# Kernel tuning notes

Measured on AMD Instinct MI355X. Metric: run time of the kernel, lower is better.

The kernel has to match this reference:

```python
import jax, jax.numpy as jnp
import numpy as np

D = 1024          # n_embd
H = 4 * D         # SwiGLU hidden
E = 8             # num_experts
K = 2             # top_k
B, T = 2, 2048

def setup_inputs() -> dict:
    key = jax.random.key(0)
    ks = jax.random.split(key, 12)
    s = 0.02
    return {
        "x":   jax.random.normal(ks[0], (B, T, D), jnp.float32),
        "noise": jax.random.normal(ks[1], (B, T, E), jnp.float32),
        # router (nn.Linear with bias=True by default)
        "Wr": jax.random.normal(ks[2], (D, E), jnp.float32) * s,
        "br": jnp.zeros((E,), jnp.float32),
        "Wn": jax.random.normal(ks[3], (D, E), jnp.float32) * s,
        "bn": jnp.zeros((E,), jnp.float32),
        # routed experts, stacked over E (bias=False)
        "Wg": jax.random.normal(ks[4], (E, D, H), jnp.float32) * s,
        "Wu": jax.random.normal(ks[5], (E, D, H), jnp.float32) * s,
        "Wd": jax.random.normal(ks[6], (E, H, D), jnp.float32) * s,
        # shared expert (num_shared_experts = 1)
        "Sg": jax.random.normal(ks[7], (D, H), jnp.float32) * s,
        "Su": jax.random.normal(ks[8], (D, H), jnp.float32) * s,
        "Sd": jax.random.normal(ks[9], (H, D), jnp.float32) * s,
    }

def reference(x, noise, Wr, br, Wn, bn, Wg, Wu, Wd, Sg, Su, Sd):
    # shared expert: SwiGLU MLP over all tokens
    shared_out = (jax.nn.silu(x @ Sg) * (x @ Su)) @ Sd  # [B,T,D]

    # noisy top-k router
    logits = x @ Wr + br                                 # [B,T,E]
    noise_logits = x @ Wn + bn
    noisy = logits + noise * jax.nn.softplus(noise_logits)
    _, top_idx = jax.lax.top_k(noisy, K)                 # [B,T,K]
    sel = jax.nn.one_hot(top_idx, E, dtype=noisy.dtype).sum(-2) > 0  # [B,T,E]
    sparse = jnp.where(sel, noisy, -jnp.inf)
    gates = jax.nn.softmax(sparse, axis=-1)              # [B,T,E], 0 for unselected

    # original runs every expert densely over all tokens, weighted by gate
    g = jnp.einsum('btd,edh->beth', x, Wg)               # [B,E,T,H]
    u = jnp.einsum('btd,edh->beth', x, Wu)
    y = jnp.einsum('beth,ehd->betd', jax.nn.silu(g) * u, Wd)  # [B,E,T,D]
    routed = jnp.einsum('bte,betd->btd', gates, y)

    return shared_out + routed
```

## Files before the change

kernel.cpp:

```cpp
#include <hip/hip_runtime.h>

typedef unsigned short u16;
typedef unsigned int u32;
typedef __attribute__((ext_vector_type(8))) __bf16 bf16x8;
typedef __attribute__((ext_vector_type(4))) float f32x4;

#define D_ 1024
#define H_ 4096
#define E_ 8
#define NT_ 4096
#define RCAP_ 8704

#define LDSH_ 8192
#define LDST_ 16384


__device__ __forceinline__ u16 f2b(float f) {
  u32 u = __float_as_uint(f);
  u += 0x7fffu + ((u >> 16) & 1u);
  return (u16)(u >> 16);
}

__device__ __forceinline__ void glds16(const u16* g, u16* l) {
  __builtin_amdgcn_global_load_lds((const __attribute__((address_space(1))) void*)g,
                                   (__attribute__((address_space(3))) void*)l, 16, 0, 0);
}

__device__ __forceinline__ void stage_half(const u16* __restrict__ g, u16* l, int wv, int lane) {
#pragma unroll
  for (int c = 0; c < 2; ++c)
    glds16(g + c * 4096 + wv * 512 + lane * 8, l + c * 4096 + wv * 512);
}

__global__ void init_ints(int* p, int n) {
  int i = threadIdx.x;
  if (i < n) p[i] = 0;
}

__global__ void pack_x(const float* __restrict__ x, u16* __restrict__ xp) {
  const int t = blockIdx.x, i = threadIdx.x;
  float4 v = ((const float4*)(x + (size_t)t * D_))[i];
  const int kb = i >> 4, ch = (i >> 1) & 7, sub = (i & 1) * 4;
  u16 tmp[4] = {f2b(v.x), f2b(v.y), f2b(v.z), f2b(v.w)};
  *(uint2*)(xp + ((size_t)kb * NT_ + t) * 64 + ((ch ^ (t & 7)) << 3) + sub) = *(uint2*)tmp;
}

__global__ void pack_b(const float* __restrict__ src, const float* __restrict__ src2,
                       u16* __restrict__ dst, int Kdim, int Rdim) {
  const int r0 = blockIdx.x * 64, k0 = blockIdx.y * 64, z = blockIdx.z;
  const int Rout = src2 ? (Rdim * 2) : Rdim;
  src += (size_t)z * Kdim * Rdim;
  if (src2) src2 += (size_t)z * Kdim * Rdim;
  u16* dkb = dst + (size_t)z * (Kdim >> 6) * Rout * 64 + (size_t)(k0 >> 6) * Rout * 64;
  __shared__ float t1[64][65];
  __shared__ float t2[64][65];
  const int tx = threadIdx.x, ty = threadIdx.y;
#pragma unroll
  for (int i = 0; i < 16; ++i) {
    const int kk = ty + 4 * i;
    t1[kk][tx] = src[(size_t)(k0 + kk) * Rdim + r0 + tx];
    if (src2) t2[kk][tx] = src2[(size_t)(k0 + kk) * Rdim + r0 + tx];
  }
  __syncthreads();
  const int idx = ty * 64 + tx;
  const int ch = idx & 7, rl0 = idx >> 3;
#pragma unroll
  for (int half = 0; half < 2; ++half) {
    const int rl = rl0 + 32 * half;
    const int r = r0 + rl;
    if (src2) {
      const int rg = 32 * (r >> 4) + (r & 15), ru = rg + 16;
      const int kg = (ch ^ (rg & 7)) << 3;
      union { u16 v[8]; uint4 q; } pg, pu;
#pragma unroll
      for (int j = 0; j < 8; ++j) pg.v[j] = f2b(t1[kg + j][rl]);
#pragma unroll
      for (int j = 0; j < 8; ++j) pu.v[j] = f2b(t2[kg + j][rl]);
      *(uint4*)(dkb + (size_t)rg * 64 + ch * 8) = pg.q;
      *(uint4*)(dkb + (size_t)ru * 64 + ch * 8) = pu.q;
    } else {
      const int kc = (ch ^ (r & 7)) << 3;
      union { u16 v[8]; uint4 q; } pk;
#pragma unroll
      for (int j = 0; j < 8; ++j) pk.v[j] = f2b(t1[kc + j][rl]);
      *(uint4*)(dkb + (size_t)r * 64 + ch * 8) = pk.q;
    }
  }
}

__global__ void router_k(const float* __restrict__ x, const float* __restrict__ noise,
                         const float* __restrict__ Wr, const float* __restrict__ br,
                         const float* __restrict__ Wn, const float* __restrict__ bn,
                         int* __restrict__ counts, int* __restrict__ tok_e,
                         float* __restrict__ tok_g) {
  const int t = blockIdx.x;
  const int lane = threadIdx.x;
  float xv[16];
#pragma unroll
  for (int i = 0; i < 16; ++i) xv[i] = x[(size_t)t * D_ + lane + 64 * i];
  float nz[E_];
#pragma unroll
  for (int e = 0; e < E_; ++e) {
    float ar = 0.f, an = 0.f;
#pragma unroll
    for (int i = 0; i < 16; ++i) {
      int d = lane + 64 * i;
      ar += xv[i] * Wr[d * E_ + e];
      an += xv[i] * Wn[d * E_ + e];
    }
#pragma unroll
    for (int o = 32; o > 0; o >>= 1) {
      ar += __shfl_down(ar, o, 64);
      an += __shfl_down(an, o, 64);
    }
    if (lane == 0) {
      float lg = ar + br[e], nl = an + bn[e];
      float sp = (nl > 20.f) ? nl : log1pf(expf(nl));
      nz[e] = lg + noise[(size_t)t * E_ + e] * sp;
    }
  }
  if (lane == 0) {
    int i0 = 0;
#pragma unroll
    for (int e = 1; e < E_; ++e) if (nz[e] > nz[i0]) i0 = e;
    int i1 = (i0 == 0) ? 1 : 0;
#pragma unroll
    for (int e = 0; e < E_; ++e) if (e != i0 && nz[e] > nz[i1]) i1 = e;
    float a = nz[i0], b = nz[i1];
    float m = fmaxf(a, b);
    float ea = expf(a - m), eb = expf(b - m);
    float inv = 1.f / (ea + eb);
    tok_e[2 * t] = i0; tok_e[2 * t + 1] = i1;
    tok_g[2 * t] = ea * inv; tok_g[2 * t + 1] = eb * inv;
    atomicAdd(&counts[i0], 1);
    atomicAdd(&counts[i1], 1);
  }
}

__global__ void scan_k(const int* __restrict__ counts, int* __restrict__ offsets) {
  if (threadIdx.x == 0) {
    int acc = 0;
    for (int e = 0; e < E_; ++e) { offsets[e] = acc; acc += (counts[e] + 7) & ~7; }
    offsets[E_] = acc;
  }
}

__global__ void gather_k(const u16* __restrict__ xp, const int* __restrict__ tok_e,
                         const float* __restrict__ tok_g, const int* __restrict__ offsets,
                         int* __restrict__ cursors, u16* __restrict__ Xallp,
                         int* __restrict__ row_token, float* __restrict__ row_gate) {
  const int t = blockIdx.x;
  __shared__ int rws[2];
  if (threadIdx.x < 2) {
    int e = tok_e[2 * t + threadIdx.x];
    int r = offsets[e] + atomicAdd(&cursors[e], 1);
    row_token[r] = t;
    row_gate[r] = tok_g[2 * t + threadIdx.x];
    rws[threadIdx.x] = r;
  }
  __syncthreads();
  const int r0 = rws[0], r1 = rws[1];
  const int x7 = t & 7;
#pragma unroll
  for (int it = 0; it < 2; ++it) {
    const int u = threadIdx.x + 64 * it;
    const int kb = u >> 3, cs = u & 7;
    uint4 v = *(const uint4*)(xp + ((size_t)kb * NT_ + t) * 64 + (cs << 3));
    const int c = cs ^ x7;
    *(uint4*)(Xallp + ((size_t)kb * RCAP_ + r0) * 64 + ((c ^ (r0 & 7)) << 3)) = v;
    *(uint4*)(Xallp + ((size_t)kb * RCAP_ + r1) * 64 + ((c ^ (r1 & 7)) << 3)) = v;
  }
}

__device__ __forceinline__ void gemm_core8(
    const u16* __restrict__ A, const u16* __restrict__ B,
    size_t aKS, size_t bKS, int NKB,
    u16* As, u16* Bs, f32x4 acc[8][4], int tid) {
  const int lane = tid & 63, wv = tid >> 6;
  const int wr = wv >> 2, wc = wv & 3;
  const int lm = lane & 15, lq = lane >> 4;
  const int c0 = ((lq ^ (lm & 7)) << 4);
  const char* asr = (const char*)As + (wr * 128 + lm) * 128;
  const char* bsr = (const char*)Bs + (wc * 64 + lm) * 128;

  stage_half(A,         As,         wv, lane);
  stage_half(A + LDSH_, As + LDSH_, wv, lane);
  stage_half(B,         Bs,         wv, lane);
  stage_half(B + LDSH_, Bs + LDSH_, wv, lane);
  stage_half(A + aKS,   As + LDST_, wv, lane);
  asm volatile("s_waitcnt vmcnt(2)" ::: "memory");
  __builtin_amdgcn_s_barrier();
  __builtin_amdgcn_sched_barrier(0);

  for (int t = 0; t < NKB; ++t) {
    const int bo = (t & 1) << 15;
    const int ou = ((t & 1) ^ 1) * LDST_;
    bf16x8 a[8], bb[4];
#pragma unroll
    for (int i = 0; i < 8; ++i)
      a[i] = *(const bf16x8*)(asr + bo + i * 2048 + c0);
#pragma unroll
    for (int j = 0; j < 4; ++j)
      bb[j] = *(const bf16x8*)(bsr + bo + j * 2048 + c0);
    if (t + 1 < NKB) stage_half(A + (size_t)(t + 1) * aKS + LDSH_, As + ou + LDSH_, wv, lane);
    asm volatile("s_waitcnt lgkmcnt(8)" ::: "memory");
    __builtin_amdgcn_s_barrier();
    asm volatile("s_waitcnt lgkmcnt(0)" ::: "memory");
    __builtin_amdgcn_sched_barrier(0);
    __builtin_amdgcn_s_setprio(1);
#pragma unroll
    for (int i = 0; i < 4; ++i)
#pragma unroll
      for (int j = 0; j < 4; ++j)
        acc[i][j] = __builtin_amdgcn_mfma_f32_16x16x32_bf16(a[i], bb[j], acc[i][j], 0, 0, 0);
    __builtin_amdgcn_s_setprio(0);
    __builtin_amdgcn_s_barrier();
    if (t + 1 < NKB) stage_half(B + (size_t)(t + 1) * bKS, Bs + ou, wv, lane);
    __builtin_amdgcn_s_barrier();
    __builtin_amdgcn_sched_barrier(0);
    __builtin_amdgcn_s_setprio(1);
#pragma unroll
    for (int i = 0; i < 4; ++i)
#pragma unroll
      for (int j = 0; j < 4; ++j)
        acc[4 + i][j] = __builtin_amdgcn_mfma_f32_16x16x32_bf16(a[4 + i], bb[j], acc[4 + i][j], 0, 0, 0);
    __builtin_amdgcn_s_setprio(0);
    __builtin_amdgcn_s_barrier();
#pragma unroll
    for (int i = 0; i < 8; ++i)
      a[i] = *(const bf16x8*)(asr + bo + i * 2048 + (c0 ^ 64));
#pragma unroll
    for (int j = 0; j < 4; ++j)
      bb[j] = *(const bf16x8*)(bsr + bo + j * 2048 + (c0 ^ 64));
    if (t + 1 < NKB) stage_half(B + (size_t)(t + 1) * bKS + LDSH_, Bs + ou + LDSH_, wv, lane);
    asm volatile("s_waitcnt lgkmcnt(8)" ::: "memory");
    __builtin_amdgcn_s_barrier();
    asm volatile("s_waitcnt lgkmcnt(0)" ::: "memory");
    __builtin_amdgcn_sched_barrier(0);
    __builtin_amdgcn_s_setprio(1);
#pragma unroll
    for (int i = 0; i < 4; ++i)
#pragma unroll
      for (int j = 0; j < 4; ++j)
        acc[i][j] = __builtin_amdgcn_mfma_f32_16x16x32_bf16(a[i], bb[j], acc[i][j], 0, 0, 0);
    __builtin_amdgcn_s_setprio(0);
    __builtin_amdgcn_s_barrier();
    if (t + 2 < NKB) stage_half(A + (size_t)(t + 2) * aKS, As + (bo >> 1), wv, lane);
    __builtin_amdgcn_s_barrier();
    __builtin_amdgcn_sched_barrier(0);
    __builtin_amdgcn_s_setprio(1);
#pragma unroll
    for (int i = 0; i < 4; ++i)
#pragma unroll
      for (int j = 0; j < 4; ++j)
        acc[4 + i][j] = __builtin_amdgcn_mfma_f32_16x16x32_bf16(a[4 + i], bb[j], acc[4 + i][j], 0, 0, 0);
    __builtin_amdgcn_s_setprio(0);
    if (t + 1 < NKB) {
      if (t + 2 < NKB) { asm volatile("s_waitcnt vmcnt(2)" ::: "memory"); }
      else             { asm volatile("s_waitcnt vmcnt(0)" ::: "memory"); }
      __builtin_amdgcn_sched_barrier(0);
      __builtin_amdgcn_s_barrier();
    }
  }
}

__global__ __launch_bounds__(512, 2)
void gemm1_k(const u16* __restrict__ Ap, const u16* __restrict__ Bp, u16* __restrict__ actp,
             const int* __restrict__ neArr, const int* __restrict__ offArr,
             int fixedM, int K, int aRowCap) {
  int bx, by, e;
  if (neArr) {
    const int lid = blockIdx.x + (int)gridDim.x * (blockIdx.y + (int)gridDim.y * blockIdx.z);
    e = lid & 7; const int rest = lid >> 3; bx = rest & 15; by = rest >> 4;
  } else { bx = blockIdx.x; by = blockIdx.y; e = 0; }
  const int ne = neArr ? neArr[e] : fixedM;
  const int m0 = bx * 256;
  if (m0 >= ne) return;
  const int off = offArr ? offArr[e] : 0;
  const int n0 = by * 256;
  const int NKB = K >> 6;
  const u16* A = Ap + (size_t)(off + m0) * 64;
  const u16* B = Bp + ((size_t)e * NKB * 8192 + (size_t)n0) * 64;

  __shared__ __align__(16) u16 As[2 * LDST_], Bs[2 * LDST_];
  f32x4 acc[8][4] = {};
  const int tid = threadIdx.x;
  gemm_core8(A, B, (size_t)aRowCap * 64, (size_t)8192 * 64, NKB, As, Bs, acc, tid);

  const int lane = tid & 63, wv = tid >> 6;
  const int wr = wv >> 2, wc = wv & 3;
  const int lm = lane & 15, lq = lane >> 4;
  const int hb = (n0 + wc * 64) >> 1;
#pragma unroll
  for (int i = 0; i < 8; ++i)
#pragma unroll
    for (int r = 0; r < 4; ++r) {
      const int m = m0 + wr * 128 + i * 16 + lq * 4 + r;
      if (m < ne) {
        const int row = off + m;
        const int r7 = row & 7;
#pragma unroll
        for (int jj = 0; jj < 2; ++jj) {
          float g = acc[i][2 * jj][r], u = acc[i][2 * jj + 1][r];
          float s = g / (1.f + __expf(-g)) * u;
          const int h = hb + jj * 16 + lm;
          actp[((size_t)(h >> 6) * RCAP_ + row) * 64 + ((((h >> 3) & 7) ^ r7) << 3 | (h & 7))] = f2b(s);
        }
      }
    }
}

__global__ __launch_bounds__(512, 2)
void gemm2_k(const u16* __restrict__ Ap, const u16* __restrict__ Bp,
             float* __restrict__ out,
             const int* __restrict__ neArr, const int* __restrict__ offArr,
             const int* __restrict__ row_token, const float* __restrict__ row_gate,
             int fixedM, int K) {
  int bx, by, e;
  if (neArr) {
    const int lid = blockIdx.x + (int)gridDim.x * (blockIdx.y + (int)gridDim.y * blockIdx.z);
    e = lid & 7; const int rest = lid >> 3; bx = rest & 15; by = rest >> 4;
  } else { bx = blockIdx.x; by = blockIdx.y; e = 0; }
  const int ne = neArr ? neArr[e] : fixedM;
  const int m0 = bx * 256;
  if (m0 >= ne) return;
  const int off = offArr ? offArr[e] : 0;
  const int n0 = by * 256;
  const int NKB = K >> 6;
  const u16* A = Ap + (size_t)(off + m0) * 64;
  const u16* B = Bp + ((size_t)e * NKB * 1024 + (size_t)n0) * 64;

  __shared__ __align__(16) u16 As[2 * LDST_], Bs[2 * LDST_];
  f32x4 acc[8][4] = {};
  const int tid = threadIdx.x;
  gemm_core8(A, B, (size_t)RCAP_ * 64, (size_t)1024 * 64, NKB, As, Bs, acc, tid);

  const int lane = tid & 63, wv = tid >> 6;
  const int wr = wv >> 2, wc = wv & 3;
  const int lm = lane & 15, lq = lane >> 4;
#pragma unroll
  for (int i = 0; i < 8; ++i)
#pragma unroll
    for (int r = 0; r < 4; ++r) {
      const int m = m0 + wr * 128 + i * 16 + lq * 4 + r;
      if (m < ne) {
        const int n = n0 + wc * 64 + lm;
        if (row_token) {
          const int tkn = row_token[off + m];
          const float gt = row_gate[off + m];
#pragma unroll
          for (int j = 0; j < 4; ++j)
            atomicAdd(out + (size_t)tkn * D_ + n + j * 16, gt * acc[i][j][r]);
        } else {
#pragma unroll
          for (int j = 0; j < 4; ++j)
            out[(size_t)m * D_ + n + j * 16] = acc[i][j][r];
        }
      }
    }
}

extern "C" void kernel_launch(void* const* d_in, const int* in_sizes, int n_in,
                              void* d_out, int out_size, void* d_ws, size_t ws_size,
                              hipStream_t stream) {
  const float* x     = (const float*)d_in[0];
  const float* noise = (const float*)d_in[1];
  const float* Wr    = (const float*)d_in[2];
  const float* br    = (const float*)d_in[3];
  const float* Wn    = (const float*)d_in[4];
  const float* bn    = (const float*)d_in[5];
  const float* Wg    = (const float*)d_in[6];
  const float* Wu    = (const float*)d_in[7];
  const float* Wd    = (const float*)d_in[8];
  const float* Sg    = (const float*)d_in[9];
  const float* Su    = (const float*)d_in[10];
  const float* Sd    = (const float*)d_in[11];
  float* out = (float*)d_out;

  char* base = (char*)d_ws;
  size_t off = 0;
  auto take = [&](size_t bytes) -> void* {
    void* r = base + off;
    off = (off + bytes + 255) & ~(size_t)255;
    return r;
  };
  u16* Wgup = (u16*)take((size_t)E_ * 16 * 8192 * 64 * 2);
  u16* Wdp  = (u16*)take((size_t)E_ * 64 * 1024 * 64 * 2);
  u16* Sgup = (u16*)take((size_t)16 * 8192 * 64 * 2);
  u16* Sdp  = (u16*)take((size_t)64 * 1024 * 64 * 2);
  u16* xp   = (u16*)take((size_t)16 * NT_ * 64 * 2);
  u16* Xallp = (u16*)take((size_t)16 * RCAP_ * 64 * 2);
  u16* actp  = (u16*)take((size_t)64 * RCAP_ * 64 * 2);
  int*   row_token = (int*)take(RCAP_ * 4);
  float* row_gate  = (float*)take(RCAP_ * 4);
  int*   tok_e = (int*)take(NT_ * 2 * 4);
  float* tok_g = (float*)take(NT_ * 2 * 4);
  int* ints = (int*)take(32 * 4);
  int* counts = ints, *cursors = ints + 8, *offsets = ints + 16;
  if (off > ws_size) return;

  hipLaunchKernelGGL(init_ints, dim3(1), dim3(64), 0, stream, ints, 32);
  hipLaunchKernelGGL(pack_x, dim3(NT_), dim3(256), 0, stream, x, xp);
  dim3 tb(64, 4);
  hipLaunchKernelGGL(pack_b, dim3(H_ / 64, D_ / 64, E_), tb, 0, stream, Wg, Wu, Wgup, D_, H_);
  hipLaunchKernelGGL(pack_b, dim3(D_ / 64, H_ / 64, E_), tb, 0, stream,
                     Wd, (const float*)nullptr, Wdp, H_, D_);
  hipLaunchKernelGGL(pack_b, dim3(H_ / 64, D_ / 64, 1), tb, 0, stream, Sg, Su, Sgup, D_, H_);
  hipLaunchKernelGGL(pack_b, dim3(D_ / 64, H_ / 64, 1), tb, 0, stream,
                     Sd, (const float*)nullptr, Sdp, H_, D_);

  hipLaunchKernelGGL(router_k, dim3(NT_), dim3(64), 0, stream,
                     x, noise, Wr, br, Wn, bn, counts, tok_e, tok_g);
  hipLaunchKernelGGL(scan_k, dim3(1), dim3(64), 0, stream, counts, offsets);
  hipLaunchKernelGGL(gather_k, dim3(NT_), dim3(64), 0, stream,
                     xp, tok_e, tok_g, offsets, cursors, Xallp, row_token, row_gate);

  hipLaunchKernelGGL(gemm1_k, dim3(16, 32, 1), dim3(512), 0, stream,
                     xp, Sgup, actp, (const int*)nullptr, (const int*)nullptr, NT_, D_, NT_);
  hipLaunchKernelGGL(gemm2_k, dim3(16, 4, 1), dim3(512), 0, stream,
                     actp, Sdp, out, (const int*)nullptr, (const int*)nullptr,
                     (const int*)nullptr, (const float*)nullptr, NT_, H_);
  hipLaunchKernelGGL(gemm1_k, dim3(16, 32, E_), dim3(512), 0, stream,
                     Xallp, Wgup, actp, counts, offsets, 0, D_, RCAP_);
  hipLaunchKernelGGL(gemm2_k, dim3(16, 4, E_), dim3(512), 0, stream,
                     actp, Wdp, out, counts, offsets, row_token, row_gate, 0, H_);
}
```

Baseline: 1.537 ms.

## Merge shared and routed expert GEMMs into single launches and restage pipeline

Shared-expert and routed-expert rows now live in one combined activation buffer (shared tokens first, routed rows after), so gemm1 and gemm2 each run as a single launch. This drops two launches and the tail/idle gaps between them. The shared output is now accumulated with atomics into a zero-initialised output, which costs an extra zero pass and more atomic traffic. The GEMM core also changes its prefetch: it stages the full A+B tile two k-steps ahead in one burst and issues 32 MFMAs per phase instead of interleaving half-tile loads between 16-MFMA groups, which reduces barriers.

```diff
diff --git a/kernel.cpp b/kernel.cpp
--- a/kernel.cpp
+++ b/kernel.cpp
@@ -10,6 +10,7 @@
 #define E_ 8
 #define NT_ 4096
 #define RCAP_ 8704
+#define CAPX_ 12800
 
 #define LDSH_ 8192
 #define LDST_ 16384
@@ -32,17 +33,29 @@
     glds16(g + c * 4096 + wv * 512 + lane * 8, l + c * 4096 + wv * 512);
 }
 
+__device__ __forceinline__ void stage_tile(const u16* __restrict__ ga, const u16* __restrict__ gb,
+                                           u16* la, u16* lb, int wv, int lane) {
+  stage_half(ga,         la,         wv, lane);
+  stage_half(ga + LDSH_, la + LDSH_, wv, lane);
+  stage_half(gb,         lb,         wv, lane);
+  stage_half(gb + LDSH_, lb + LDSH_, wv, lane);
+}
+
 __global__ void init_ints(int* p, int n) {
   int i = threadIdx.x;
   if (i < n) p[i] = 0;
 }
 
-__global__ void pack_x(const float* __restrict__ x, u16* __restrict__ xp) {
+__global__ void zero_f32(float* __restrict__ p) {
+  ((float4*)p)[blockIdx.x * 256 + threadIdx.x] = make_float4(0.f, 0.f, 0.f, 0.f);
+}
+
+__global__ void pack_x(const float* __restrict__ x, u16* __restrict__ xc) {
   const int t = blockIdx.x, i = threadIdx.x;
   float4 v = ((const float4*)(x + (size_t)t * D_))[i];
   const int kb = i >> 4, ch = (i >> 1) & 7, sub = (i & 1) * 4;
   u16 tmp[4] = {f2b(v.x), f2b(v.y), f2b(v.z), f2b(v.w)};
-  *(uint2*)(xp + ((size_t)kb * NT_ + t) * 64 + ((ch ^ (t & 7)) << 3) + sub) = *(uint2*)tmp;
+  *(uint2*)(xc + ((size_t)kb * CAPX_ + t) * 64 + ((ch ^ (t & 7)) << 3) + sub) = *(uint2*)tmp;
 }
 
 __global__ void pack_b(const float* __restrict__ src, const float* __restrict__ src2,
@@ -145,9 +158,9 @@
   }
 }
 
-__global__ void gather_k(const u16* __restrict__ xp, const int* __restrict__ tok_e,
+__global__ void gather_k(const u16* __restrict__ xc, const int* __restrict__ tok_e,
                          const float* __restrict__ tok_g, const int* __restrict__ offsets,
-                         int* __restrict__ cursors, u16* __restrict__ Xallp,
+                         int* __restrict__ cursors, u16* __restrict__ xcw,
                          int* __restrict__ row_token, float* __restrict__ row_gate) {
   const int t = blockIdx.x;
   __shared__ int rws[2];
@@ -165,10 +178,10 @@
   for (int it = 0; it < 2; ++it) {
     const int u = threadIdx.x + 64 * it;
     const int kb = u >> 3, cs = u & 7;
-    uint4 v = *(const uint4*)(xp + ((size_t)kb * NT_ + t) * 64 + (cs << 3));
+    uint4 v = *(const uint4*)(xc + ((size_t)kb * CAPX_ + t) * 64 + (cs << 3));
     const int c = cs ^ x7;
-    *(uint4*)(Xallp + ((size_t)kb * RCAP_ + r0) * 64 + ((c ^ (r0 & 7)) << 3)) = v;
-    *(uint4*)(Xallp + ((size_t)kb * RCAP_ + r1) * 64 + ((c ^ (r1 & 7)) << 3)) = v;
+    *(uint4*)(xcw + ((size_t)kb * CAPX_ + NT_ + r0) * 64 + ((c ^ (r0 & 7)) << 3)) = v;
+    *(uint4*)(xcw + ((size_t)kb * CAPX_ + NT_ + r1) * 64 + ((c ^ (r1 & 7)) << 3)) = v;
   }
 }
 
@@ -183,18 +196,15 @@
   const char* asr = (const char*)As + (wr * 128 + lm) * 128;
   const char* bsr = (const char*)Bs + (wc * 64 + lm) * 128;
 
-  stage_half(A,         As,         wv, lane);
-  stage_half(A + LDSH_, As + LDSH_, wv, lane);
-  stage_half(B,         Bs,         wv, lane);
-  stage_half(B + LDSH_, Bs + LDSH_, wv, lane);
-  stage_half(A + aKS,   As + LDST_, wv, lane);
-  asm volatile("s_waitcnt vmcnt(2)" ::: "memory");
+  stage_tile(A, B, As, Bs, wv, lane);
+  stage_tile(A + aKS, B + bKS, As + LDST_, Bs + LDST_, wv, lane);
+  asm volatile("s_waitcnt vmcnt(8)" ::: "memory");
   __builtin_amdgcn_s_barrier();
   __builtin_amdgcn_sched_barrier(0);
 
   for (int t = 0; t < NKB; ++t) {
-    const int bo = (t & 1) << 15;
-    const int ou = ((t & 1) ^ 1) * LDST_;
+    const int bu = (t & 1) * LDST_;
+    const int bo = bu * 2;
     bf16x8 a[8], bb[4];
 #pragma unroll
     for (int i = 0; i < 8; ++i)
@@ -202,61 +212,40 @@
 #pragma unroll
     for (int j = 0; j < 4; ++j)
       bb[j] = *(const bf16x8*)(bsr + bo + j * 2048 + c0);
-    if (t + 1 < NKB) stage_half(A + (size_t)(t + 1) * aKS + LDSH_, As + ou + LDSH_, wv, lane);
     asm volatile("s_waitcnt lgkmcnt(8)" ::: "memory");
     __builtin_amdgcn_s_barrier();
     asm volatile("s_waitcnt lgkmcnt(0)" ::: "memory");
     __builtin_amdgcn_sched_barrier(0);
     __builtin_amdgcn_s_setprio(1);
 #pragma unroll
-    for (int i = 0; i < 4; ++i)
+    for (int i = 0; i < 8; ++i)
 #pragma unroll
       for (int j = 0; j < 4; ++j)
         acc[i][j] = __builtin_amdgcn_mfma_f32_16x16x32_bf16(a[i], bb[j], acc[i][j], 0, 0, 0);
     __builtin_amdgcn_s_setprio(0);
     __builtin_amdgcn_s_barrier();
-    if (t + 1 < NKB) stage_half(B + (size_t)(t + 1) * bKS, Bs + ou, wv, lane);
-    __builtin_amdgcn_s_barrier();
-    __builtin_amdgcn_sched_barrier(0);
-    __builtin_amdgcn_s_setprio(1);
-#pragma unroll
-    for (int i = 0; i < 4; ++i)
-#pragma unroll
-      for (int j = 0; j < 4; ++j)
-        acc[4 + i][j] = __builtin_amdgcn_mfma_f32_16x16x32_bf16(a[4 + i], bb[j], acc[4 + i][j], 0, 0, 0);
-    __builtin_amdgcn_s_setprio(0);
-    __builtin_amdgcn_s_barrier();
 #pragma unroll
     for (int i = 0; i < 8; ++i)
       a[i] = *(const bf16x8*)(asr + bo + i * 2048 + (c0 ^ 64));
 #pragma unroll
     for (int j = 0; j < 4; ++j)
       bb[j] = *(const bf16x8*)(bsr + bo + j * 2048 + (c0 ^ 64));
-    if (t + 1 < NKB) stage_half(B + (size_t)(t + 1) * bKS + LDSH_, Bs + ou + LDSH_, wv, lane);
     asm volatile("s_waitcnt lgkmcnt(8)" ::: "memory");
     __builtin_amdgcn_s_barrier();
     asm volatile("s_waitcnt lgkmcnt(0)" ::: "memory");
     __builtin_amdgcn_sched_barrier(0);
+    if (t + 2 < NKB)
+      stage_tile(A + (size_t)(t + 2) * aKS, B + (size_t)(t + 2) * bKS,
+                 As + bu, Bs + bu, wv, lane);
     __builtin_amdgcn_s_setprio(1);
 #pragma unroll
-    for (int i = 0; i < 4; ++i)
+    for (int i = 0; i < 8; ++i)
 #pragma unroll
       for (int j = 0; j < 4; ++j)
         acc[i][j] = __builtin_amdgcn_mfma_f32_16x16x32_bf16(a[i], bb[j], acc[i][j], 0, 0, 0);
     __builtin_amdgcn_s_setprio(0);
-    __builtin_amdgcn_s_barrier();
-    if (t + 2 < NKB) stage_half(A + (size_t)(t + 2) * aKS, As + (bo >> 1), wv, lane);
-    __builtin_amdgcn_s_barrier();
-    __builtin_amdgcn_sched_barrier(0);
-    __builtin_amdgcn_s_setprio(1);
-#pragma unroll
-    for (int i = 0; i < 4; ++i)
-#pragma unroll
-      for (int j = 0; j < 4; ++j)
-        acc[4 + i][j] = __builtin_amdgcn_mfma_f32_16x16x32_bf16(a[4 + i], bb[j], acc[4 + i][j], 0, 0, 0);
-    __builtin_amdgcn_s_setprio(0);
     if (t + 1 < NKB) {
-      if (t + 2 < NKB) { asm volatile("s_waitcnt vmcnt(2)" ::: "memory"); }
+      if (t + 2 < NKB) { asm volatile("s_waitcnt vmcnt(8)" ::: "memory"); }
       else             { asm volatile("s_waitcnt vmcnt(0)" ::: "memory"); }
       __builtin_amdgcn_sched_barrier(0);
       __builtin_amdgcn_s_barrier();
@@ -265,27 +254,33 @@
 }
 
 __global__ __launch_bounds__(512, 2)
-void gemm1_k(const u16* __restrict__ Ap, const u16* __restrict__ Bp, u16* __restrict__ actp,
-             const int* __restrict__ neArr, const int* __restrict__ offArr,
-             int fixedM, int K, int aRowCap) {
-  int bx, by, e;
-  if (neArr) {
-    const int lid = blockIdx.x + (int)gridDim.x * (blockIdx.y + (int)gridDim.y * blockIdx.z);
-    e = lid & 7; const int rest = lid >> 3; bx = rest & 15; by = rest >> 4;
-  } else { bx = blockIdx.x; by = blockIdx.y; e = 0; }
-  const int ne = neArr ? neArr[e] : fixedM;
-  const int m0 = bx * 256;
-  if (m0 >= ne) return;
-  const int off = offArr ? offArr[e] : 0;
-  const int n0 = by * 256;
-  const int NKB = K >> 6;
-  const u16* A = Ap + (size_t)(off + m0) * 64;
-  const u16* B = Bp + ((size_t)e * NKB * 8192 + (size_t)n0) * 64;
+void gemm1_k(const u16* __restrict__ XC, const u16* __restrict__ Wgup,
+             const u16* __restrict__ Sgup, u16* __restrict__ ACT,
+             const int* __restrict__ counts, const int* __restrict__ offsets) {
+  const int lid = blockIdx.x;
+  int rowbase, mrem, n0;
+  const u16* B;
+  if (lid < 4096) {
+    const int e = lid & 7, bx = (lid >> 3) & 15, by = lid >> 7;
+    const int ne = counts[e];
+    if (bx * 256 >= ne) return;
+    mrem = ne - bx * 256;
+    rowbase = NT_ + offsets[e] + bx * 256;
+    n0 = by * 256;
+    B = Wgup + ((size_t)e * 16 * 8192 + n0) * 64;
+  } else {
+    const int s = lid - 4096, bx = s & 15, by = s >> 4;
+    mrem = 256;
+    rowbase = bx * 256;
+    n0 = by * 256;
+    B = Sgup + (size_t)n0 * 64;
+  }
+  const u16* A = XC + (size_t)rowbase * 64;
 
   __shared__ __align__(16) u16 As[2 * LDST_], Bs[2 * LDST_];
   f32x4 acc[8][4] = {};
   const int tid = threadIdx.x;
-  gemm_core8(A, B, (size_t)aRowCap * 64, (size_t)8192 * 64, NKB, As, Bs, acc, tid);
+  gemm_core8(A, B, (size_t)CAPX_ * 64, (size_t)8192 * 64, D_ >> 6, As, Bs, acc, tid);
 
   const int lane = tid & 63, wv = tid >> 6;
   const int wr = wv >> 2, wc = wv & 3;
@@ -294,46 +289,55 @@
 #pragma unroll
   for (int i = 0; i < 8; ++i)
 #pragma unroll
-    for (int r = 0; r < 4; ++r) {
-      const int m = m0 + wr * 128 + i * 16 + lq * 4 + r;
-      if (m < ne) {
-        const int row = off + m;
+    for (int q = 0; q < 4; ++q) {
+      const int m = wr * 128 + i * 16 + lq * 4 + q;
+      if (m < mrem) {
+        const int row = rowbase + m;
         const int r7 = row & 7;
 #pragma unroll
         for (int jj = 0; jj < 2; ++jj) {
-          float g = acc[i][2 * jj][r], u = acc[i][2 * jj + 1][r];
+          float g = acc[i][2 * jj][q], u = acc[i][2 * jj + 1][q];
           float s = g / (1.f + __expf(-g)) * u;
           const int h = hb + jj * 16 + lm;
-          actp[((size_t)(h >> 6) * RCAP_ + row) * 64 + ((((h >> 3) & 7) ^ r7) << 3 | (h & 7))] = f2b(s);
+          ACT[((size_t)(h >> 6) * CAPX_ + row) * 64 + ((((h >> 3) & 7) ^ r7) << 3 | (h & 7))] = f2b(s);
         }
       }
     }
 }
 
 __global__ __launch_bounds__(512, 2)
-void gemm2_k(const u16* __restrict__ Ap, const u16* __restrict__ Bp,
-             float* __restrict__ out,
-             const int* __restrict__ neArr, const int* __restrict__ offArr,
-             const int* __restrict__ row_token, const float* __restrict__ row_gate,
-             int fixedM, int K) {
-  int bx, by, e;
-  if (neArr) {
-    const int lid = blockIdx.x + (int)gridDim.x * (blockIdx.y + (int)gridDim.y * blockIdx.z);
-    e = lid & 7; const int rest = lid >> 3; bx = rest & 15; by = rest >> 4;
-  } else { bx = blockIdx.x; by = blockIdx.y; e = 0; }
-  const int ne = neArr ? neArr[e] : fixedM;
-  const int m0 = bx * 256;
-  if (m0 >= ne) return;
-  const int off = offArr ? offArr[e] : 0;
-  const int n0 = by * 256;
-  const int NKB = K >> 6;
-  const u16* A = Ap + (size_t)(off + m0) * 64;
-  const u16* B = Bp + ((size_t)e * NKB * 1024 + (size_t)n0) * 64;
+void gemm2_k(const u16* __restrict__ ACT, const u16* __restrict__ Wdp,
+             const u16* __restrict__ Sdp, float* __restrict__ out,
+             const int* __restrict__ counts, const int* __restrict__ offsets,
+             const int* __restrict__ row_token, const float* __restrict__ row_gate) {
+  const int lid = blockIdx.x;
+  int rowbase, mrem, n0;
+  bool routed;
+  const u16* B;
+  if (lid < 512) {
+    const int e = lid & 7, r = lid >> 3;
+    const int bx = r & 15, by = r >> 4;
+    const int ne = counts[e];
+    if (bx * 256 >= ne) return;
+    mrem = ne - bx * 256;
+    rowbase = NT_ + offsets[e] + bx * 256;
+    n0 = by * 256;
+    B = Wdp + ((size_t)e * 64 * 1024 + n0) * 64;
+    routed = true;
+  } else {
+    const int s = lid - 512, bx = s & 15, by = s >> 4;
+    mrem = 256;
+    rowbase = bx * 256;
+    n0 = by * 256;
+    B = Sdp + (size_t)n0 * 64;
+    routed = false;
+  }
+  const u16* A = ACT + (size_t)rowbase * 64;
 
   __shared__ __align__(16) u16 As[2 * LDST_], Bs[2 * LDST_];
   f32x4 acc[8][4] = {};
   const int tid = threadIdx.x;
-  gemm_core8(A, B, (size_t)RCAP_ * 64, (size_t)1024 * 64, NKB, As, Bs, acc, tid);
+  gemm_core8(A, B, (size_t)CAPX_ * 64, (size_t)1024 * 64, H_ >> 6, As, Bs, acc, tid);
 
   const int lane = tid & 63, wv = tid >> 6;
   const int wr = wv >> 2, wc = wv & 3;
@@ -341,21 +345,17 @@
 #pragma unroll
   for (int i = 0; i < 8; ++i)
 #pragma unroll
-    for (int r = 0; r < 4; ++r) {
-      const int m = m0 + wr * 128 + i * 16 + lq * 4 + r;
-      if (m < ne) {
+    for (int q = 0; q < 4; ++q) {
+      const int m = wr * 128 + i * 16 + lq * 4 + q;
+      if (m < mrem) {
+        const int rowAbs = rowbase + m;
+        int tkn; float gt;
+        if (routed) { const int idx = rowAbs - NT_; tkn = row_token[idx]; gt = row_gate[idx]; }
+        else        { tkn = rowAbs; gt = 1.f; }
         const int n = n0 + wc * 64 + lm;
-        if (row_token) {
-          const int tkn = row_token[off + m];
-          const float gt = row_gate[off + m];
-#pragma unroll
-          for (int j = 0; j < 4; ++j)
-            atomicAdd(out + (size_t)tkn * D_ + n + j * 16, gt * acc[i][j][r]);
-        } else {
-#pragma unroll
-          for (int j = 0; j < 4; ++j)
-            out[(size_t)m * D_ + n + j * 16] = acc[i][j][r];
-        }
+#pragma unroll
+        for (int j = 0; j < 4; ++j)
+          atomicAdd(out + (size_t)tkn * D_ + n + j * 16, gt * acc[i][j][q]);
       }
     }
 }
@@ -388,9 +388,8 @@
   u16* Wdp  = (u16*)take((size_t)E_ * 64 * 1024 * 64 * 2);
   u16* Sgup = (u16*)take((size_t)16 * 8192 * 64 * 2);
   u16* Sdp  = (u16*)take((size_t)64 * 1024 * 64 * 2);
-  u16* xp   = (u16*)take((size_t)16 * NT_ * 64 * 2);
-  u16* Xallp = (u16*)take((size_t)16 * RCAP_ * 64 * 2);
-  u16* actp  = (u16*)take((size_t)64 * RCAP_ * 64 * 2);
+  u16* XC   = (u16*)take((size_t)16 * CAPX_ * 64 * 2);
+  u16* ACT  = (u16*)take((size_t)64 * CAPX_ * 64 * 2);
   int*   row_token = (int*)take(RCAP_ * 4);
   float* row_gate  = (float*)take(RCAP_ * 4);
   int*   tok_e = (int*)take(NT_ * 2 * 4);
@@ -400,7 +399,8 @@
   if (off > ws_size) return;
 
   hipLaunchKernelGGL(init_ints, dim3(1), dim3(64), 0, stream, ints, 32);
-  hipLaunchKernelGGL(pack_x, dim3(NT_), dim3(256), 0, stream, x, xp);
+  hipLaunchKernelGGL(zero_f32, dim3(NT_ * D_ / 4 / 256), dim3(256), 0, stream, out);
+  hipLaunchKernelGGL(pack_x, dim3(NT_), dim3(256), 0, stream, x, XC);
   dim3 tb(64, 4);
   hipLaunchKernelGGL(pack_b, dim3(H_ / 64, D_ / 64, E_), tb, 0, stream, Wg, Wu, Wgup, D_, H_);
   hipLaunchKernelGGL(pack_b, dim3(D_ / 64, H_ / 64, E_), tb, 0, stream,
@@ -413,15 +413,10 @@
                      x, noise, Wr, br, Wn, bn, counts, tok_e, tok_g);
   hipLaunchKernelGGL(scan_k, dim3(1), dim3(64), 0, stream, counts, offsets);
   hipLaunchKernelGGL(gather_k, dim3(NT_), dim3(64), 0, stream,
-                     xp, tok_e, tok_g, offsets, cursors, Xallp, row_token, row_gate);
-
-  hipLaunchKernelGGL(gemm1_k, dim3(16, 32, 1), dim3(512), 0, stream,
-                     xp, Sgup, actp, (const int*)nullptr, (const int*)nullptr, NT_, D_, NT_);
-  hipLaunchKernelGGL(gemm2_k, dim3(16, 4, 1), dim3(512), 0, stream,
-                     actp, Sdp, out, (const int*)nullptr, (const int*)nullptr,
-                     (const int*)nullptr, (const float*)nullptr, NT_, H_);
-  hipLaunchKernelGGL(gemm1_k, dim3(16, 32, E_), dim3(512), 0, stream,
-                     Xallp, Wgup, actp, counts, offsets, 0, D_, RCAP_);
-  hipLaunchKernelGGL(gemm2_k, dim3(16, 4, E_), dim3(512), 0, stream,
-                     actp, Wdp, out, counts, offsets, row_token, row_gate, 0, H_);
-}
+                     XC, tok_e, tok_g, offsets, cursors, XC, row_token, row_gate);
+
+  hipLaunchKernelGGL(gemm1_k, dim3(4096 + 512), dim3(512), 0, stream,
+                     XC, Wgup, Sgup, ACT, counts, offsets);
+  hipLaunchKernelGGL(gemm2_k, dim3(512 + 64), dim3(512), 0, stream,
+                     ACT, Wdp, Sdp, out, counts, offsets, row_token, row_gate);
+}
```

Result: no change. 1.538 ms (+0.1%).
